# Kernel optimization log

Hardware: AMD Instinct MI355X
Metric: run time of the kernel (lower is better)

Reference implementation:

```python
import jax, jax.numpy as jnp
import numpy as np

DN = ('NCDHW', 'OIDHW', 'NCDHW')

def conv3d(x, w, b):
    # kernel 3, padding 1, stride 1 -> SAME
    y = jax.lax.conv_general_dilated(x, w, window_strides=(1, 1, 1), padding='SAME', dimension_numbers=DN)
    return y + b[None, :, None, None, None]

def setup_inputs() -> dict:
    key = jax.random.key(0)
    ks = jax.random.split(key, 7)
    C, Cqk = 64, 8  # in_channels, in_channels // 8
    x = jax.random.normal(ks[0], (2, C, 20, 20, 20), dtype=jnp.float32)
    fan_qk = C * 27
    fan_v = C * 27
    wq = jax.random.normal(ks[1], (Cqk, C, 3, 3, 3), dtype=jnp.float32) / np.sqrt(fan_qk)
    bq = jax.random.normal(ks[2], (Cqk,), dtype=jnp.float32) * 0.01
    wk = jax.random.normal(ks[3], (Cqk, C, 3, 3, 3), dtype=jnp.float32) / np.sqrt(fan_qk)
    bk = jax.random.normal(ks[4], (Cqk,), dtype=jnp.float32) * 0.01
    wv = jax.random.normal(ks[5], (C, C, 3, 3, 3), dtype=jnp.float32) / np.sqrt(fan_v)
    bv = jax.random.normal(ks[6], (C,), dtype=jnp.float32) * 0.01
    return {'x': x, 'wq': wq, 'bq': bq, 'wk': wk, 'bk': bk, 'wv': wv, 'bv': bv}

def reference(x, wq, bq, wk, bk, wv, bv):
    b, C, h, w, d = x.shape
    n = h * w * d
    M = conv3d(x, wq, bq).reshape(b, -1, n)   # (b, C/8, n)
    N = conv3d(x, wk, bk).reshape(b, -1, n)   # (b, C/8, n)
    V = conv3d(x, wv, bv).reshape(b, C, n)    # (b, C, n)
    # B[b,i,j] = softmax_j( sum_c M[b,c,i] * N[b,c,j] )  (no scale factor, as in source)
    scores = jnp.einsum('bci,bcj->bij', M, N)
    B = jax.nn.softmax(scores, axis=-1)
    # GSA[b,c,i] = sum_j V[b,c,j] * B[b,i,j]
    out = jnp.einsum('bcj,bij->bci', V, B).reshape(b, C, h, w, d)
    return out
```

## Files before the change

### kernel.cpp

```cpp
#include <hip/hip_runtime.h>
#include <hip/hip_bf16.h>
#include <math.h>

#define NSP 8000
#define CIN 64
#define LOG2E 1.4426950408889634f

typedef __attribute__((ext_vector_type(8)))  short    bf16x8;
typedef __attribute__((ext_vector_type(4)))  float    f32x4;
typedef __attribute__((ext_vector_type(16))) float    f32x16;
typedef __attribute__((ext_vector_type(8)))  _Float16 f16x8;
typedef __attribute__((ext_vector_type(2)))  __fp16   fp16x2;

__device__ __forceinline__ ushort f2bf(float f) {
    unsigned u = __float_as_uint(f);
    unsigned r = (u + 0x7fffu + ((u >> 16) & 1u)) >> 16;
    return (ushort)r;
}

__global__ __launch_bounds__(64) void prep_kernel(
    const float* __restrict__ wq, const float* __restrict__ wk,
    const float* __restrict__ wv, const float* __restrict__ x,
    ushort* __restrict__ wtap, ushort* __restrict__ xpad)
{
    const int bid = blockIdx.x;
    if (bid < 2160) {
        const int tap = bid / 80;
        const int co  = bid % 80;
        const int ci  = threadIdx.x;
        float v;
        if (co < 8)       v = wq[(co * 64 + ci) * 27 + tap];
        else if (co < 16) v = wk[((co - 8) * 64 + ci) * 27 + tap];
        else              v = wv[((co - 16) * 64 + ci) * 27 + tap];
        wtap[((size_t)tap * 80 + co) * 64 + ci] = f2bf(v);
    } else {
        const int bx  = bid - 2160;
        const int b   = bx / 484;
        const int rem = bx % 484;
        const int zp  = rem / 22, yp = rem % 22;
        const int ci  = threadIdx.x;
        const bool zy = (zp >= 1 && zp <= 20) && (yp >= 1 && yp <= 20);
        const float* xb = x + ((size_t)b * 64 + ci) * NSP + (zp - 1) * 400 + (yp - 1) * 20;
        ushort* op = xpad + (size_t)b * 681472 + (size_t)(zp * 484 + yp * 22) * 64 + ci;
        #pragma unroll
        for (int xp = 0; xp < 22; ++xp) {
            float v = 0.0f;
            if (zy && xp >= 1 && xp <= 20) v = xb[xp - 1];
            op[xp * 64] = f2bf(v);
        }
    }
}

__global__ __launch_bounds__(512, 2) void conv_mfma_kernel(
    const ushort* __restrict__ xpad, const ushort* __restrict__ wtap,
    const float* __restrict__ bq, const float* __restrict__ bk,
    const float* __restrict__ bv,
    _Float16* __restrict__ Qt, _Float16* __restrict__ Kt, _Float16* __restrict__ VT)
{
    const int t  = threadIdx.x;
    const int l  = t & 63;
    const int w  = t >> 6;
    const int st = w & 1;
    const int sp = w >> 1;
    const int bx = blockIdx.x * 2 + st;
    const int b  = blockIdx.y;
    const int s  = bx * 16 + (l & 15);
    const int z  = s / 400;
    const int r0 = s % 400;
    const int y  = r0 / 20;
    const int xx = r0 % 20;
    const int kq = (l >> 4) * 8;

    const ushort* xb = xpad + (size_t)b * 681472
                     + (size_t)(z * 484 + y * 22 + xx) * 64 + kq;
    const ushort* wl = wtap + (l & 15) * 64 + kq;

    f32x4 acc[5];
    #pragma unroll
    for (int ct = 0; ct < 5; ++ct) acc[ct] = (f32x4)0.0f;

    const int tap0 = sp * 7;
    const int tap1 = (sp == 3) ? 27 : (tap0 + 7);

    for (int tap = tap0; tap < tap1; ++tap) {
        const int dz = tap / 9;
        const int r9 = tap % 9;
        const int dy = r9 / 3;
        const int dx = r9 % 3;
        const ushort* xp2 = xb + (size_t)(dz * 484 + dy * 22 + dx) * 64;
        const bf16x8 b0 = *(const bf16x8*)(xp2);
        const bf16x8 b1 = *(const bf16x8*)(xp2 + 32);
        const ushort* wp = wl + (size_t)tap * 80 * 64;
        #pragma unroll
        for (int ct = 0; ct < 5; ++ct) {
            const bf16x8 a0 = *(const bf16x8*)(wp + ct * 16 * 64);
            const bf16x8 a1 = *(const bf16x8*)(wp + ct * 16 * 64 + 32);
            acc[ct] = __builtin_amdgcn_mfma_f32_16x16x32_bf16(a0, b0, acc[ct], 0, 0, 0);
            acc[ct] = __builtin_amdgcn_mfma_f32_16x16x32_bf16(a1, b1, acc[ct], 0, 0, 0);
        }
    }

    __shared__ float lacc[3][2][64][20];
    if (sp > 0) {
        #pragma unroll
        for (int ct = 0; ct < 5; ++ct)
            *(f32x4*)&lacc[sp - 1][st][l][ct * 4] = acc[ct];
    }
    __syncthreads();
    if (sp == 0) {
        #pragma unroll
        for (int ct = 0; ct < 5; ++ct) {
            #pragma unroll
            for (int r = 0; r < 4; ++r) {
                const float v = acc[ct][r] + lacc[0][st][l][ct * 4 + r]
                             + lacc[1][st][l][ct * 4 + r] + lacc[2][st][l][ct * 4 + r];
                const int co = ct * 16 + (l >> 4) * 4 + r;
                if (co < 8)
                    Qt[((size_t)b * NSP + s) * 8 + co] = (_Float16)((v + bq[co]) * LOG2E);
                else if (co < 16)
                    Kt[((size_t)b * NSP + s) * 8 + (co - 8)] = (_Float16)(v + bk[co - 8]);
                else {
                    const int c = co - 16;
                    VT[(size_t)b * 512000 + ((size_t)bx * 64 + c) * 16 + (l & 15)] =
                        (_Float16)(v + bv[c]);
                }
            }
        }
    }
}

__global__ __launch_bounds__(512, 2) void attn_kernel(
    const _Float16* __restrict__ Qt, const _Float16* __restrict__ Kt,
    const _Float16* __restrict__ VT, float* __restrict__ out)
{
    const int t  = threadIdx.x;
    const int l  = t & 63;
    const int w  = t >> 6;
    const int b  = blockIdx.y;
    const int i0 = blockIdx.x * 32;
    const int il = l & 31;
    const int hi = l >> 5;

    const _Float16* Qtb = Qt + (size_t)b * NSP * 8;
    const _Float16* Ktb = Kt + (size_t)b * NSP * 8;
    const _Float16* VTb = VT + (size_t)b * 512000;

    __shared__ __align__(16) char smem[34816];
    float* mrg = (float*)smem;
    float* mml = (float*)(smem + 32768);
    float* lsm = (float*)(smem + 33792);

    f16x8 qf = (f16x8)(_Float16)0.0f;
    if (l < 32) qf = *(const f16x8*)&Qtb[(size_t)(i0 + il) * 8];

    float m = -INFINITY, lsum = 0.0f;
    f32x16 acc0 = (f32x16)0.0f, acc1 = (f32x16)0.0f;
    const f32x16 zero16 = (f32x16)0.0f;

#define LOADK(JT, KF) { KF = (f16x8)(_Float16)0.0f;                         \
        if (l < 32) KF = *(const f16x8*)&Ktb[(size_t)((JT) * 32 + il) * 8]; }
#define LOADV(JT, VF) { const int jb = (JT) * 2;                            \
        VF##00 = *(const f16x8*)&VTb[((size_t)(jb + 0) * 64 + il) * 16 + 8 * hi];      \
        VF##01 = *(const f16x8*)&VTb[((size_t)(jb + 1) * 64 + il) * 16 + 8 * hi];      \
        VF##10 = *(const f16x8*)&VTb[((size_t)(jb + 0) * 64 + 32 + il) * 16 + 8 * hi]; \
        VF##11 = *(const f16x8*)&VTb[((size_t)(jb + 1) * 64 + 32 + il) * 16 + 8 * hi]; }

    int jt = w;
    f16x8 kf, vf00, vf01, vf10, vf11;
    LOADK(jt, kf);
    LOADV(jt, vf);

    while (jt < 250) {
        const int jn = jt + 8;
        const bool has = (jn < 250);
        f16x8 kf_n, vn00, vn01, vn10, vn11;
        if (has) { LOADK(jn, kf_n); LOADV(jn, vn); }

        f32x16 sacc = __builtin_amdgcn_mfma_f32_32x32x16_f16(kf, qf, zero16, 0, 0, 0);

        float x0 = fmaxf(sacc[0], sacc[1]),   x1 = fmaxf(sacc[2], sacc[3]);
        float x2 = fmaxf(sacc[4], sacc[5]),   x3 = fmaxf(sacc[6], sacc[7]);
        float x4 = fmaxf(sacc[8], sacc[9]),   x5 = fmaxf(sacc[10], sacc[11]);
        float x6 = fmaxf(sacc[12], sacc[13]), x7 = fmaxf(sacc[14], sacc[15]);
        float pm = fmaxf(fmaxf(fmaxf(x0, x1), fmaxf(x2, x3)),
                         fmaxf(fmaxf(x4, x5), fmaxf(x6, x7)));

        if (__any(pm > m + 8.0f)) {
            pm = fmaxf(pm, __shfl_xor(pm, 32));
            const float mn = fmaxf(m, pm);
            const float sc = __builtin_amdgcn_exp2f(m - mn);
            #pragma unroll
            for (int r = 0; r < 16; ++r) { acc0[r] *= sc; acc1[r] *= sc; }
            lsum *= sc;
            m = mn;
        }

        #pragma unroll
        for (int r = 0; r < 16; ++r)
            sacc[r] = __builtin_amdgcn_exp2f(sacc[r] - m);
        {
            float s0 = (sacc[0] + sacc[1]) + (sacc[2] + sacc[3]);
            float s1 = (sacc[4] + sacc[5]) + (sacc[6] + sacc[7]);
            float s2 = (sacc[8] + sacc[9]) + (sacc[10] + sacc[11]);
            float s3 = (sacc[12] + sacc[13]) + (sacc[14] + sacc[15]);
            lsum += (s0 + s1) + (s2 + s3);
        }

        unsigned w0, w1, w2, w3, w4, w5, w6, w7;
        {
            union { fp16x2 h; unsigned u; } c;
            c.h = __builtin_amdgcn_cvt_pkrtz(sacc[0],  sacc[1]);  w0 = c.u;
            c.h = __builtin_amdgcn_cvt_pkrtz(sacc[2],  sacc[3]);  w1 = c.u;
            c.h = __builtin_amdgcn_cvt_pkrtz(sacc[4],  sacc[5]);  w2 = c.u;
            c.h = __builtin_amdgcn_cvt_pkrtz(sacc[6],  sacc[7]);  w3 = c.u;
            c.h = __builtin_amdgcn_cvt_pkrtz(sacc[8],  sacc[9]);  w4 = c.u;
            c.h = __builtin_amdgcn_cvt_pkrtz(sacc[10], sacc[11]); w5 = c.u;
            c.h = __builtin_amdgcn_cvt_pkrtz(sacc[12], sacc[13]); w6 = c.u;
            c.h = __builtin_amdgcn_cvt_pkrtz(sacc[14], sacc[15]); w7 = c.u;
        }
        unsigned A0 = w0, A2 = w2, A1 = w1, A3 = w3;
        unsigned B0 = w4, B2 = w6, B1 = w5, B3 = w7;
        asm("v_permlane32_swap_b32 %0, %1" : "+v"(A0), "+v"(A2));
        asm("v_permlane32_swap_b32 %0, %1" : "+v"(A1), "+v"(A3));
        asm("v_permlane32_swap_b32 %0, %1" : "+v"(B0), "+v"(B2));
        asm("v_permlane32_swap_b32 %0, %1" : "+v"(B1), "+v"(B3));
        union { unsigned u[4]; f16x8 v; } pf0u, pf1u;
        pf0u.u[0] = A0; pf0u.u[1] = A1; pf0u.u[2] = A2; pf0u.u[3] = A3;
        pf1u.u[0] = B0; pf1u.u[1] = B1; pf1u.u[2] = B2; pf1u.u[3] = B3;

        __builtin_amdgcn_s_setprio(1);
        acc0 = __builtin_amdgcn_mfma_f32_32x32x16_f16(vf00, pf0u.v, acc0, 0, 0, 0);
        acc1 = __builtin_amdgcn_mfma_f32_32x32x16_f16(vf10, pf0u.v, acc1, 0, 0, 0);
        acc0 = __builtin_amdgcn_mfma_f32_32x32x16_f16(vf01, pf1u.v, acc0, 0, 0, 0);
        acc1 = __builtin_amdgcn_mfma_f32_32x32x16_f16(vf11, pf1u.v, acc1, 0, 0, 0);
        __builtin_amdgcn_s_setprio(0);

        if (has) {
            kf = kf_n;
            vf00 = vn00; vf01 = vn01; vf10 = vn10; vf11 = vn11;
        }
        jt = jn;
    }
#undef LOADK
#undef LOADV

    lsum += __shfl_xor(lsum, 32);
    if (l < 32) mml[w * 32 + il] = m;
    __syncthreads();
    float gm = mml[il];
    #pragma unroll
    for (int ww = 1; ww < 8; ++ww) gm = fmaxf(gm, mml[ww * 32 + il]);
    const float f = __builtin_amdgcn_exp2f(m - gm);
    if (l < 32) lsm[w * 32 + il] = lsum * f;
    #pragma unroll
    for (int r = 0; r < 16; ++r) { acc0[r] *= f; acc1[r] *= f; }

    float* ob = out + (size_t)b * 64 * NSP + i0;

    #pragma unroll
    for (int r = 0; r < 16; ++r) {
        const int cl = (r & 3) + 8 * (r >> 2) + 4 * hi;
        mrg[w * 1024 + cl * 32 + il] = acc0[r];
    }
    __syncthreads();
    #pragma unroll
    for (int rep = 0; rep < 2; ++rep) {
        const int e = t + rep * 512;
        const int c = e >> 5, i = e & 31;
        float sv = 0.0f, lg = 0.0f;
        #pragma unroll
        for (int ww = 0; ww < 8; ++ww) {
            sv += mrg[ww * 1024 + c * 32 + i];
            lg += lsm[ww * 32 + i];
        }
        float inv;
        asm("v_rcp_f32 %0, %1" : "=v"(inv) : "v"(lg));
        ob[(size_t)c * NSP + i] = sv * inv;
    }
    __syncthreads();

    #pragma unroll
    for (int r = 0; r < 16; ++r) {
        const int cl = (r & 3) + 8 * (r >> 2) + 4 * hi;
        mrg[w * 1024 + cl * 32 + il] = acc1[r];
    }
    __syncthreads();
    #pragma unroll
    for (int rep = 0; rep < 2; ++rep) {
        const int e = t + rep * 512;
        const int c = e >> 5, i = e & 31;
        float sv = 0.0f, lg = 0.0f;
        #pragma unroll
        for (int ww = 0; ww < 8; ++ww) {
            sv += mrg[ww * 1024 + c * 32 + i];
            lg += lsm[ww * 32 + i];
        }
        float inv;
        asm("v_rcp_f32 %0, %1" : "=v"(inv) : "v"(lg));
        ob[(size_t)(32 + c) * NSP + i] = sv * inv;
    }
}

extern "C" void kernel_launch(void* const* d_in, const int* in_sizes, int n_in,
                              void* d_out, int out_size, void* d_ws, size_t ws_size,
                              hipStream_t stream) {
    const float* x  = (const float*)d_in[0];
    const float* wq = (const float*)d_in[1];
    const float* bq = (const float*)d_in[2];
    const float* wk = (const float*)d_in[3];
    const float* bk = (const float*)d_in[4];
    const float* wv = (const float*)d_in[5];
    const float* bv = (const float*)d_in[6];
    float* out = (float*)d_out;

    ushort*   wtap = (ushort*)d_ws;
    ushort*   xpad = (ushort*)((char*)d_ws + 278528);
    _Float16* Qt   = (_Float16*)((char*)d_ws + 3004416);
    _Float16* Kt   = (_Float16*)((char*)d_ws + 3260416);
    _Float16* VT   = (_Float16*)((char*)d_ws + 3516416);

    prep_kernel<<<dim3(3128), 64, 0, stream>>>(wq, wk, wv, x, wtap, xpad);
    conv_mfma_kernel<<<dim3(250, 2), 512, 0, stream>>>(xpad, wtap, bq, bk, bv, Qt, Kt, VT);
    attn_kernel<<<dim3(250, 2), 512, 0, stream>>>(Qt, Kt, VT, out);
}
```

Before: 152.6 us.

## Reuse conv weights across two spatial tiles and compute softmax row sums via MFMA

The conv kernel now has each wave process two 16-position spatial tiles, so every weight fragment is loaded once and used for both. The tap loops are fully unrolled and the grid is halved. In the attention kernel, the per-lane scalar sum of exponentials is replaced by extra MFMAs against a ones vector, moving that reduction onto the matrix units. This adds two MFMAs per tile and more registers, and occupancy may drop now that the min-blocks launch bound is removed from the conv kernel.

```diff
diff --git a/kernel.cpp b/kernel.cpp
--- a/kernel.cpp
+++ b/kernel.cpp
@@ -51,7 +51,7 @@
     }
 }
 
-__global__ __launch_bounds__(512, 2) void conv_mfma_kernel(
+__global__ __launch_bounds__(512) void conv_mfma_kernel(
     const ushort* __restrict__ xpad, const ushort* __restrict__ wtap,
     const float* __restrict__ bq, const float* __restrict__ bk,
     const float* __restrict__ bv,
@@ -62,67 +62,84 @@
     const int w  = t >> 6;
     const int st = w & 1;
     const int sp = w >> 1;
-    const int bx = blockIdx.x * 2 + st;
     const int b  = blockIdx.y;
-    const int s  = bx * 16 + (l & 15);
-    const int z  = s / 400;
-    const int r0 = s % 400;
-    const int y  = r0 / 20;
-    const int xx = r0 % 20;
+    const int s0 = blockIdx.x * 64 + st * 32;
     const int kq = (l >> 4) * 8;
 
-    const ushort* xb = xpad + (size_t)b * 681472
-                     + (size_t)(z * 484 + y * 22 + xx) * 64 + kq;
-    const ushort* wl = wtap + (l & 15) * 64 + kq;
-
-    f32x4 acc[5];
-    #pragma unroll
-    for (int ct = 0; ct < 5; ++ct) acc[ct] = (f32x4)0.0f;
-
-    const int tap0 = sp * 7;
-    const int tap1 = (sp == 3) ? 27 : (tap0 + 7);
-
-    for (int tap = tap0; tap < tap1; ++tap) {
-        const int dz = tap / 9;
-        const int r9 = tap % 9;
-        const int dy = r9 / 3;
-        const int dx = r9 % 3;
-        const ushort* xp2 = xb + (size_t)(dz * 484 + dy * 22 + dx) * 64;
-        const bf16x8 b0 = *(const bf16x8*)(xp2);
-        const bf16x8 b1 = *(const bf16x8*)(xp2 + 32);
-        const ushort* wp = wl + (size_t)tap * 80 * 64;
+    const int sA = s0 + (l & 15);
+    const int sB = sA + 16;
+    const int zA = sA / 400, rA = sA % 400, yA = rA / 20, xA = rA % 20;
+    const int zB = sB / 400, rB = sB % 400, yB = rB / 20, xB = rB % 20;
+
+    const ushort* xpb = xpad + (size_t)b * 681472;
+    const ushort* xbA = xpb + (size_t)(zA * 484 + yA * 22 + xA) * 64 + kq;
+    const ushort* xbB = xpb + (size_t)(zB * 484 + yB * 22 + xB) * 64 + kq;
+    const ushort* wl  = wtap + (l & 15) * 64 + kq;
+
+    f32x4 accA[5], accB[5];
+    #pragma unroll
+    for (int ct = 0; ct < 5; ++ct) { accA[ct] = (f32x4)0.0f; accB[ct] = (f32x4)0.0f; }
+
+#define TAP(TAPI) {                                                          \
+        const int tap_ = (TAPI);                                             \
+        const int dz_ = tap_ / 9, r9_ = tap_ % 9;                            \
+        const int off_ = (dz_ * 484 + (r9_ / 3) * 22 + (r9_ % 3)) * 64;      \
+        const bf16x8 bA0 = *(const bf16x8*)(xbA + off_);                     \
+        const bf16x8 bA1 = *(const bf16x8*)(xbA + off_ + 32);                \
+        const bf16x8 bB0 = *(const bf16x8*)(xbB + off_);                     \
+        const bf16x8 bB1 = *(const bf16x8*)(xbB + off_ + 32);                \
+        const ushort* wp_ = wl + (size_t)tap_ * 80 * 64;                     \
+        _Pragma("unroll") for (int ct = 0; ct < 5; ++ct) {                   \
+            const bf16x8 a0 = *(const bf16x8*)(wp_ + ct * 16 * 64);          \
+            const bf16x8 a1 = *(const bf16x8*)(wp_ + ct * 16 * 64 + 32);     \
+            accA[ct] = __builtin_amdgcn_mfma_f32_16x16x32_bf16(a0, bA0, accA[ct], 0, 0, 0); \
+            accA[ct] = __builtin_amdgcn_mfma_f32_16x16x32_bf16(a1, bA1, accA[ct], 0, 0, 0); \
+            accB[ct] = __builtin_amdgcn_mfma_f32_16x16x32_bf16(a0, bB0, accB[ct], 0, 0, 0); \
+            accB[ct] = __builtin_amdgcn_mfma_f32_16x16x32_bf16(a1, bB1, accB[ct], 0, 0, 0); \
+        } }
+
+    if (sp < 3) {
+        const int tap0 = sp * 7;
+        #pragma unroll
+        for (int k = 0; k < 7; ++k) TAP(tap0 + k);
+    } else {
+        #pragma unroll
+        for (int k = 0; k < 6; ++k) TAP(21 + k);
+    }
+#undef TAP
+
+    __shared__ float lacc[3][2][2][64][20];
+    if (sp > 0) {
         #pragma unroll
         for (int ct = 0; ct < 5; ++ct) {
-            const bf16x8 a0 = *(const bf16x8*)(wp + ct * 16 * 64);
-            const bf16x8 a1 = *(const bf16x8*)(wp + ct * 16 * 64 + 32);
-            acc[ct] = __builtin_amdgcn_mfma_f32_16x16x32_bf16(a0, b0, acc[ct], 0, 0, 0);
-            acc[ct] = __builtin_amdgcn_mfma_f32_16x16x32_bf16(a1, b1, acc[ct], 0, 0, 0);
-        }
-    }
-
-    __shared__ float lacc[3][2][64][20];
-    if (sp > 0) {
-        #pragma unroll
-        for (int ct = 0; ct < 5; ++ct)
-            *(f32x4*)&lacc[sp - 1][st][l][ct * 4] = acc[ct];
+            *(f32x4*)&lacc[sp - 1][st][0][l][ct * 4] = accA[ct];
+            *(f32x4*)&lacc[sp - 1][st][1][l][ct * 4] = accB[ct];
+        }
     }
     __syncthreads();
     if (sp == 0) {
         #pragma unroll
-        for (int ct = 0; ct < 5; ++ct) {
+        for (int u = 0; u < 2; ++u) {
+            const int s  = s0 + u * 16 + (l & 15);
+            const int jb = s >> 4;
             #pragma unroll
-            for (int r = 0; r < 4; ++r) {
-                const float v = acc[ct][r] + lacc[0][st][l][ct * 4 + r]
-                             + lacc[1][st][l][ct * 4 + r] + lacc[2][st][l][ct * 4 + r];
-                const int co = ct * 16 + (l >> 4) * 4 + r;
-                if (co < 8)
-                    Qt[((size_t)b * NSP + s) * 8 + co] = (_Float16)((v + bq[co]) * LOG2E);
-                else if (co < 16)
-                    Kt[((size_t)b * NSP + s) * 8 + (co - 8)] = (_Float16)(v + bk[co - 8]);
-                else {
-                    const int c = co - 16;
-                    VT[(size_t)b * 512000 + ((size_t)bx * 64 + c) * 16 + (l & 15)] =
-                        (_Float16)(v + bv[c]);
+            for (int ct = 0; ct < 5; ++ct) {
+                #pragma unroll
+                for (int r = 0; r < 4; ++r) {
+                    float v = (u ? accB[ct][r] : accA[ct][r]);
+                    v += lacc[0][st][u][l][ct * 4 + r]
+                       + lacc[1][st][u][l][ct * 4 + r]
+                       + lacc[2][st][u][l][ct * 4 + r];
+                    const int co = ct * 16 + (l >> 4) * 4 + r;
+                    if (co < 8)
+                        Qt[((size_t)b * NSP + s) * 8 + co] = (_Float16)((v + bq[co]) * LOG2E);
+                    else if (co < 16)
+                        Kt[((size_t)b * NSP + s) * 8 + (co - 8)] = (_Float16)(v + bk[co - 8]);
+                    else {
+                        const int c = co - 16;
+                        VT[(size_t)b * 512000 + ((size_t)jb * 64 + c) * 16 + (l & 15)] =
+                            (_Float16)(v + bv[c]);
+                    }
                 }
             }
         }
@@ -153,8 +170,12 @@
     f16x8 qf = (f16x8)(_Float16)0.0f;
     if (l < 32) qf = *(const f16x8*)&Qtb[(size_t)(i0 + il) * 8];
 
-    float m = -INFINITY, lsum = 0.0f;
-    f32x16 acc0 = (f32x16)0.0f, acc1 = (f32x16)0.0f;
+    f16x8 onesf;
+    #pragma unroll
+    for (int e = 0; e < 8; ++e) onesf[e] = (_Float16)1.0f;
+
+    float m = -INFINITY;
+    f32x16 acc0 = (f32x16)0.0f, acc1 = (f32x16)0.0f, acc2 = (f32x16)0.0f;
     const f32x16 zero16 = (f32x16)0.0f;
 
 #define LOADK(JT, KF) { KF = (f16x8)(_Float16)0.0f;                         \
@@ -178,33 +199,28 @@
 
         f32x16 sacc = __builtin_amdgcn_mfma_f32_32x32x16_f16(kf, qf, zero16, 0, 0, 0);
 
-        float x0 = fmaxf(sacc[0], sacc[1]),   x1 = fmaxf(sacc[2], sacc[3]);
-        float x2 = fmaxf(sacc[4], sacc[5]),   x3 = fmaxf(sacc[6], sacc[7]);
-        float x4 = fmaxf(sacc[8], sacc[9]),   x5 = fmaxf(sacc[10], sacc[11]);
-        float x6 = fmaxf(sacc[12], sacc[13]), x7 = fmaxf(sacc[14], sacc[15]);
-        float pm = fmaxf(fmaxf(fmaxf(x0, x1), fmaxf(x2, x3)),
-                         fmaxf(fmaxf(x4, x5), fmaxf(x6, x7)));
+        float m1 = fmaxf(fmaxf(sacc[0],  sacc[1]),  sacc[2]);
+        float m2 = fmaxf(fmaxf(sacc[3],  sacc[4]),  sacc[5]);
+        float m3 = fmaxf(fmaxf(sacc[6],  sacc[7]),  sacc[8]);
+        float m4 = fmaxf(fmaxf(sacc[9],  sacc[10]), sacc[11]);
+        float m5 = fmaxf(fmaxf(sacc[12], sacc[13]), sacc[14]);
+        float pm = fmaxf(fmaxf(fmaxf(m1, m2), fmaxf(m3, m4)),
+                         fmaxf(m5, sacc[15]));
 
         if (__any(pm > m + 8.0f)) {
             pm = fmaxf(pm, __shfl_xor(pm, 32));
             const float mn = fmaxf(m, pm);
             const float sc = __builtin_amdgcn_exp2f(m - mn);
             #pragma unroll
-            for (int r = 0; r < 16; ++r) { acc0[r] *= sc; acc1[r] *= sc; }
-            lsum *= sc;
+            for (int r = 0; r < 16; ++r) {
+                acc0[r] *= sc; acc1[r] *= sc; acc2[r] *= sc;
+            }
             m = mn;
         }
 
         #pragma unroll
         for (int r = 0; r < 16; ++r)
             sacc[r] = __builtin_amdgcn_exp2f(sacc[r] - m);
-        {
-            float s0 = (sacc[0] + sacc[1]) + (sacc[2] + sacc[3]);
-            float s1 = (sacc[4] + sacc[5]) + (sacc[6] + sacc[7]);
-            float s2 = (sacc[8] + sacc[9]) + (sacc[10] + sacc[11]);
-            float s3 = (sacc[12] + sacc[13]) + (sacc[14] + sacc[15]);
-            lsum += (s0 + s1) + (s2 + s3);
-        }
 
         unsigned w0, w1, w2, w3, w4, w5, w6, w7;
         {
@@ -231,8 +247,10 @@
         __builtin_amdgcn_s_setprio(1);
         acc0 = __builtin_amdgcn_mfma_f32_32x32x16_f16(vf00, pf0u.v, acc0, 0, 0, 0);
         acc1 = __builtin_amdgcn_mfma_f32_32x32x16_f16(vf10, pf0u.v, acc1, 0, 0, 0);
+        acc2 = __builtin_amdgcn_mfma_f32_32x32x16_f16(onesf, pf0u.v, acc2, 0, 0, 0);
         acc0 = __builtin_amdgcn_mfma_f32_32x32x16_f16(vf01, pf1u.v, acc0, 0, 0, 0);
         acc1 = __builtin_amdgcn_mfma_f32_32x32x16_f16(vf11, pf1u.v, acc1, 0, 0, 0);
+        acc2 = __builtin_amdgcn_mfma_f32_32x32x16_f16(onesf, pf1u.v, acc2, 0, 0, 0);
         __builtin_amdgcn_s_setprio(0);
 
         if (has) {
@@ -244,14 +262,13 @@
 #undef LOADK
 #undef LOADV
 
-    lsum += __shfl_xor(lsum, 32);
     if (l < 32) mml[w * 32 + il] = m;
     __syncthreads();
     float gm = mml[il];
     #pragma unroll
     for (int ww = 1; ww < 8; ++ww) gm = fmaxf(gm, mml[ww * 32 + il]);
     const float f = __builtin_amdgcn_exp2f(m - gm);
-    if (l < 32) lsm[w * 32 + il] = lsum * f;
+    if (l < 32) lsm[w * 32 + il] = acc2[0] * f;
     #pragma unroll
     for (int r = 0; r < 16; ++r) { acc0[r] *= f; acc1[r] *= f; }
 
@@ -320,6 +337,6 @@
     _Float16* VT   = (_Float16*)((char*)d_ws + 3516416);
 
     prep_kernel<<<dim3(3128), 64, 0, stream>>>(wq, wk, wv, x, wtap, xpad);
-    conv_mfma_kernel<<<dim3(250, 2), 512, 0, stream>>>(xpad, wtap, bq, bk, bv, Qt, Kt, VT);
+    conv_mfma_kernel<<<dim3(125, 2), 512, 0, stream>>>(xpad, wtap, bq, bk, bv, Qt, Kt, VT);
     attn_kernel<<<dim3(250, 2), 512, 0, stream>>>(Qt, Kt, VT, out);
 }
```

Result: faster. 143.1 us (-6.2%).

## Register-tile conv kernel over four spatial subtiles to reuse weight fragments

Applied to the files above, without the earlier changes.

Each wave in the conv kernel now computes four 16-position spatial subtiles, so every loaded weight fragment feeds four MFMA accumulator sets instead of one. The block shrinks to four waves (one per tap split) and the grid halves. Tap loops are fully unrolled per split, and the shared-memory reduction layout is reorganized accordingly. The aim is less redundant weight loading, at the cost of more accumulator registers and fewer waves in flight.

```diff
diff --git a/kernel.cpp b/kernel.cpp
--- a/kernel.cpp
+++ b/kernel.cpp
@@ -51,7 +51,7 @@
     }
 }
 
-__global__ __launch_bounds__(512, 2) void conv_mfma_kernel(
+__global__ __launch_bounds__(256) void conv_mfma_kernel(
     const ushort* __restrict__ xpad, const ushort* __restrict__ wtap,
     const float* __restrict__ bq, const float* __restrict__ bk,
     const float* __restrict__ bv,
@@ -59,70 +59,108 @@
 {
     const int t  = threadIdx.x;
     const int l  = t & 63;
-    const int w  = t >> 6;
-    const int st = w & 1;
-    const int sp = w >> 1;
-    const int bx = blockIdx.x * 2 + st;
+    const int sp = t >> 6;
     const int b  = blockIdx.y;
-    const int s  = bx * 16 + (l & 15);
-    const int z  = s / 400;
-    const int r0 = s % 400;
-    const int y  = r0 / 20;
-    const int xx = r0 % 20;
+    const int s0 = blockIdx.x * 64;
     const int kq = (l >> 4) * 8;
 
-    const ushort* xb = xpad + (size_t)b * 681472
-                     + (size_t)(z * 484 + y * 22 + xx) * 64 + kq;
+    const ushort* xpb = xpad + (size_t)b * 681472;
+    const ushort* xb0; const ushort* xb1; const ushort* xb2; const ushort* xb3;
+    {
+        const int s = s0 + (l & 15);
+        #define MKBASE(PTR, SS) { const int s_ = (SS);                       \
+            const int z_ = s_ / 400, r_ = s_ % 400, y_ = r_ / 20, x_ = r_ % 20; \
+            PTR = xpb + (size_t)(z_ * 484 + y_ * 22 + x_) * 64 + kq; }
+        MKBASE(xb0, s);
+        MKBASE(xb1, s + 16);
+        MKBASE(xb2, s + 32);
+        MKBASE(xb3, s + 48);
+        #undef MKBASE
+    }
     const ushort* wl = wtap + (l & 15) * 64 + kq;
 
-    f32x4 acc[5];
-    #pragma unroll
-    for (int ct = 0; ct < 5; ++ct) acc[ct] = (f32x4)0.0f;
-
-    const int tap0 = sp * 7;
-    const int tap1 = (sp == 3) ? 27 : (tap0 + 7);
-
-    for (int tap = tap0; tap < tap1; ++tap) {
-        const int dz = tap / 9;
-        const int r9 = tap % 9;
-        const int dy = r9 / 3;
-        const int dx = r9 % 3;
-        const ushort* xp2 = xb + (size_t)(dz * 484 + dy * 22 + dx) * 64;
-        const bf16x8 b0 = *(const bf16x8*)(xp2);
-        const bf16x8 b1 = *(const bf16x8*)(xp2 + 32);
-        const ushort* wp = wl + (size_t)tap * 80 * 64;
+    f32x4 acc0[5], acc1[5], acc2[5], acc3[5];
+    #pragma unroll
+    for (int ct = 0; ct < 5; ++ct) {
+        acc0[ct] = (f32x4)0.0f; acc1[ct] = (f32x4)0.0f;
+        acc2[ct] = (f32x4)0.0f; acc3[ct] = (f32x4)0.0f;
+    }
+
+#define TAP(TAPI) {                                                          \
+        const int tap_ = (TAPI);                                             \
+        const int dz_ = tap_ / 9, r9_ = tap_ % 9;                            \
+        const int off_ = (dz_ * 484 + (r9_ / 3) * 22 + (r9_ % 3)) * 64;      \
+        const bf16x8 b00 = *(const bf16x8*)(xb0 + off_);                     \
+        const bf16x8 b01 = *(const bf16x8*)(xb0 + off_ + 32);                \
+        const bf16x8 b10 = *(const bf16x8*)(xb1 + off_);                     \
+        const bf16x8 b11 = *(const bf16x8*)(xb1 + off_ + 32);                \
+        const bf16x8 b20 = *(const bf16x8*)(xb2 + off_);                     \
+        const bf16x8 b21 = *(const bf16x8*)(xb2 + off_ + 32);                \
+        const bf16x8 b30 = *(const bf16x8*)(xb3 + off_);                     \
+        const bf16x8 b31 = *(const bf16x8*)(xb3 + off_ + 32);                \
+        const ushort* wp_ = wl + (size_t)tap_ * 80 * 64;                     \
+        _Pragma("unroll") for (int ct = 0; ct < 5; ++ct) {                   \
+            const bf16x8 a0 = *(const bf16x8*)(wp_ + ct * 16 * 64);          \
+            const bf16x8 a1 = *(const bf16x8*)(wp_ + ct * 16 * 64 + 32);     \
+            acc0[ct] = __builtin_amdgcn_mfma_f32_16x16x32_bf16(a0, b00, acc0[ct], 0, 0, 0); \
+            acc0[ct] = __builtin_amdgcn_mfma_f32_16x16x32_bf16(a1, b01, acc0[ct], 0, 0, 0); \
+            acc1[ct] = __builtin_amdgcn_mfma_f32_16x16x32_bf16(a0, b10, acc1[ct], 0, 0, 0); \
+            acc1[ct] = __builtin_amdgcn_mfma_f32_16x16x32_bf16(a1, b11, acc1[ct], 0, 0, 0); \
+            acc2[ct] = __builtin_amdgcn_mfma_f32_16x16x32_bf16(a0, b20, acc2[ct], 0, 0, 0); \
+            acc2[ct] = __builtin_amdgcn_mfma_f32_16x16x32_bf16(a1, b21, acc2[ct], 0, 0, 0); \
+            acc3[ct] = __builtin_amdgcn_mfma_f32_16x16x32_bf16(a0, b30, acc3[ct], 0, 0, 0); \
+            acc3[ct] = __builtin_amdgcn_mfma_f32_16x16x32_bf16(a1, b31, acc3[ct], 0, 0, 0); \
+        } }
+
+    if (sp == 0) {
+        #pragma unroll
+        for (int k = 0; k < 7; ++k) TAP(k);
+    } else if (sp == 1) {
+        #pragma unroll
+        for (int k = 0; k < 7; ++k) TAP(7 + k);
+    } else if (sp == 2) {
+        #pragma unroll
+        for (int k = 0; k < 7; ++k) TAP(14 + k);
+    } else {
+        #pragma unroll
+        for (int k = 0; k < 6; ++k) TAP(21 + k);
+    }
+#undef TAP
+
+    __shared__ float lacc[3][4][5][64][4];
+    if (sp > 0) {
         #pragma unroll
         for (int ct = 0; ct < 5; ++ct) {
-            const bf16x8 a0 = *(const bf16x8*)(wp + ct * 16 * 64);
-            const bf16x8 a1 = *(const bf16x8*)(wp + ct * 16 * 64 + 32);
-            acc[ct] = __builtin_amdgcn_mfma_f32_16x16x32_bf16(a0, b0, acc[ct], 0, 0, 0);
-            acc[ct] = __builtin_amdgcn_mfma_f32_16x16x32_bf16(a1, b1, acc[ct], 0, 0, 0);
-        }
-    }
-
-    __shared__ float lacc[3][2][64][20];
-    if (sp > 0) {
-        #pragma unroll
-        for (int ct = 0; ct < 5; ++ct)
-            *(f32x4*)&lacc[sp - 1][st][l][ct * 4] = acc[ct];
+            *(f32x4*)&lacc[sp - 1][0][ct][l][0] = acc0[ct];
+            *(f32x4*)&lacc[sp - 1][1][ct][l][0] = acc1[ct];
+            *(f32x4*)&lacc[sp - 1][2][ct][l][0] = acc2[ct];
+            *(f32x4*)&lacc[sp - 1][3][ct][l][0] = acc3[ct];
+        }
     }
     __syncthreads();
     if (sp == 0) {
         #pragma unroll
-        for (int ct = 0; ct < 5; ++ct) {
+        for (int sub = 0; sub < 4; ++sub) {
+            const int s  = s0 + sub * 16 + (l & 15);
+            const int jb = s >> 4;
             #pragma unroll
-            for (int r = 0; r < 4; ++r) {
-                const float v = acc[ct][r] + lacc[0][st][l][ct * 4 + r]
-                             + lacc[1][st][l][ct * 4 + r] + lacc[2][st][l][ct * 4 + r];
-                const int co = ct * 16 + (l >> 4) * 4 + r;
-                if (co < 8)
-                    Qt[((size_t)b * NSP + s) * 8 + co] = (_Float16)((v + bq[co]) * LOG2E);
-                else if (co < 16)
-                    Kt[((size_t)b * NSP + s) * 8 + (co - 8)] = (_Float16)(v + bk[co - 8]);
-                else {
-                    const int c = co - 16;
-                    VT[(size_t)b * 512000 + ((size_t)bx * 64 + c) * 16 + (l & 15)] =
-                        (_Float16)(v + bv[c]);
+            for (int ct = 0; ct < 5; ++ct) {
+                const f32x4 base = (sub == 0) ? acc0[ct] : (sub == 1) ? acc1[ct]
+                                 : (sub == 2) ? acc2[ct] : acc3[ct];
+                #pragma unroll
+                for (int r = 0; r < 4; ++r) {
+                    float v = base[r] + lacc[0][sub][ct][l][r]
+                            + lacc[1][sub][ct][l][r] + lacc[2][sub][ct][l][r];
+                    const int co = ct * 16 + (l >> 4) * 4 + r;
+                    if (co < 8)
+                        Qt[((size_t)b * NSP + s) * 8 + co] = (_Float16)((v + bq[co]) * LOG2E);
+                    else if (co < 16)
+                        Kt[((size_t)b * NSP + s) * 8 + (co - 8)] = (_Float16)(v + bk[co - 8]);
+                    else {
+                        const int c = co - 16;
+                        VT[(size_t)b * 512000 + ((size_t)jb * 64 + c) * 16 + (l & 15)] =
+                            (_Float16)(v + bv[c]);
+                    }
                 }
             }
         }
@@ -320,6 +358,6 @@
     _Float16* VT   = (_Float16*)((char*)d_ws + 3516416);
 
     prep_kernel<<<dim3(3128), 64, 0, stream>>>(wq, wk, wv, x, wtap, xpad);
-    conv_mfma_kernel<<<dim3(250, 2), 512, 0, stream>>>(xpad, wtap, bq, bk, bv, Qt, Kt, VT);
+    conv_mfma_kernel<<<dim3(125, 2), 256, 0, stream>>>(xpad, wtap, bq, bk, bv, Qt, Kt, VT);
     attn_kernel<<<dim3(250, 2), 512, 0, stream>>>(Qt, Kt, VT, out);
 }
```

Result: faster. 135.2 us (-11.4%).
